# Optimization experiments

Hardware: AMD Instinct MI355X
Metric: run time of the kernel (lower is better)

## Reference

```python
import jax, jax.numpy as jnp
import numpy as np

LOG_2PI = 1.8378770664093453  # log(2*pi)


def setup_inputs() -> dict:
    key = jax.random.key(0)
    k1, k2 = jax.random.split(key)
    # Pij: posteriors [B, K, H, W]; positive like softmax outputs
    Pij = jax.random.uniform(k1, (4, 16, 512, 512), dtype=jnp.float32)
    # I: image [B, C=3, H, W]
    I = jax.random.uniform(k2, (4, 3, 512, 512), dtype=jnp.float32)
    return {"Pij": Pij, "I": I}


def reference(Pij, I):
    eps = 1e-5
    B, K, H, W = Pij.shape
    D = I.shape[1]  # = 3 (module hard-codes eye(3) jitter)
    Npix = H * W

    # M-step: mixture weights, per-class weighted means and covariances
    SP = jnp.sum(Pij, axis=(2, 3))            # [B, K]
    alpha = SP / Npix                          # [B, K]
    denom = (eps + SP)[..., None]              # [B, K, 1]
    mu = jnp.einsum('bchw,bkhw->bkc', I, Pij) / denom  # [B, K, D]

    # centered pixels per class: [B, K, D, H, W]
    diff = I[:, None, :, :, :] - mu[..., None, None]
    sig = jnp.einsum('bkhw,bkchw,bkdhw->bkcd', Pij, diff, diff) / denom[..., None]
    sig = sig + 1e-3 * jnp.eye(D, dtype=sig.dtype)  # jitter, matches eps_sigma

    # E-step: Gaussian log-density per pixel per class (tiny 3x3 algebra)
    siginv = jnp.linalg.inv(sig)               # [B, K, D, D]
    logdet = jnp.linalg.slogdet(sig)[1]        # [B, K]
    quad = jnp.einsum('bkchw,bkcd,bkdhw->bkhw', diff, siginv, diff)  # [B,K,H,W]
    logp = -0.5 * (D * LOG_2PI + logdet[..., None, None] + quad)

    Qij = alpha[..., None, None] * jnp.exp(logp)          # [B, K, H, W]
    Pij_new = Qij / (eps + jnp.sum(Qij, axis=1, keepdims=True))
    return Pij_new
```

## Files before the change

kernel.cpp:

```cpp
#include <hip/hip_runtime.h>
#include <math.h>

#define NPIX (512 * 512)
#define KCLS 16
#define NB   4
#define EPSF 1e-5f
#define D_LOG_2PI 1.8378770664093453

__global__ __launch_bounds__(256)
void k_stats(const float* __restrict__ P, const float* __restrict__ I,
             double* __restrict__ stats) {
    const int tid  = threadIdx.x;
    const int b    = blockIdx.y;
    const int base = blockIdx.x * 2048;
    const float* Ib = I + (size_t)b * 3 * NPIX;

    float xr[2][4], yr[2][4], zr[2][4];
#pragma unroll
    for (int it = 0; it < 2; ++it) {
        const int px = base + it * 1024 + tid * 4;
        *(float4*)xr[it] = *(const float4*)(Ib + px);
        *(float4*)yr[it] = *(const float4*)(Ib + NPIX + px);
        *(float4*)zr[it] = *(const float4*)(Ib + 2 * NPIX + px);
    }

    __shared__ float red[4][10];
    const int wave = tid >> 6, lane = tid & 63;

    for (int k = 0; k < KCLS; ++k) {
        const float* Pk = P + (size_t)(b * KCLS + k) * NPIX + base;
        float s[10];
#pragma unroll
        for (int j = 0; j < 10; ++j) s[j] = 0.f;

#pragma unroll
        for (int it = 0; it < 2; ++it) {
            float pv[4];
            *(float4*)pv = *(const float4*)(Pk + it * 1024 + tid * 4);
#pragma unroll
            for (int j = 0; j < 4; ++j) {
                const float p = pv[j];
                const float x = xr[it][j], y = yr[it][j], z = zr[it][j];
                const float px_ = p * x, py_ = p * y, pz_ = p * z;
                s[0] += p;
                s[1] += px_;      s[2] += py_;      s[3] += pz_;
                s[4] += px_ * x;  s[5] += px_ * y;  s[6] += px_ * z;
                s[7] += py_ * y;  s[8] += py_ * z;  s[9] += pz_ * z;
            }
        }
#pragma unroll
        for (int j = 0; j < 10; ++j) {
            float v = s[j];
#pragma unroll
            for (int off = 32; off > 0; off >>= 1)
                v += __shfl_down(v, off);
            if (lane == 0) red[wave][j] = v;
        }
        __syncthreads();
        if (tid < 10) {
            const float v = red[0][tid] + red[1][tid] + red[2][tid] + red[3][tid];
            atomicAdd(&stats[(size_t)(b * KCLS + k) * 10 + tid], (double)v);
        }
        __syncthreads();
    }
}

__global__ void k_params(const double* __restrict__ stats,
                         float* __restrict__ params) {
    const int idx = threadIdx.x;
    if (idx >= NB * KCLS) return;
    const double* s = stats + (size_t)idx * 10;
    const double SP    = s[0];
    const double denom = 1e-5 + SP;
    const double alpha = SP / (double)NPIX;
    const double m0 = s[1] / denom, m1 = s[2] / denom, m2 = s[3] / denom;
    const double c00 = (s[4] - 2.0 * m0 * s[1] + m0 * m0 * SP) / denom + 1e-3;
    const double c01 = (s[5] - m0 * s[2] - m1 * s[1] + m0 * m1 * SP) / denom;
    const double c02 = (s[6] - m0 * s[3] - m2 * s[1] + m0 * m2 * SP) / denom;
    const double c11 = (s[7] - 2.0 * m1 * s[2] + m1 * m1 * SP) / denom + 1e-3;
    const double c12 = (s[8] - m1 * s[3] - m2 * s[2] + m1 * m2 * SP) / denom;
    const double c22 = (s[9] - 2.0 * m2 * s[3] + m2 * m2 * SP) / denom + 1e-3;
    const double A00 = c11 * c22 - c12 * c12;
    const double A01 = c02 * c12 - c01 * c22;
    const double A02 = c01 * c12 - c02 * c11;
    const double A11 = c00 * c22 - c02 * c02;
    const double A12 = c01 * c02 - c00 * c12;
    const double A22 = c00 * c11 - c01 * c01;
    const double det = c00 * A00 + c01 * A01 + c02 * A02;
    const double coeff = alpha * exp(-0.5 * (3.0 * D_LOG_2PI + log(det)));
    float* o = params + (size_t)idx * 10;
    o[0] = (float)m0;          o[1] = (float)m1;          o[2] = (float)m2;
    o[3] = (float)(A00 / det); o[4] = (float)(A01 / det); o[5] = (float)(A02 / det);
    o[6] = (float)(A11 / det); o[7] = (float)(A12 / det); o[8] = (float)(A22 / det);
    o[9] = (float)coeff;
}

__global__ __launch_bounds__(256)
void k_estep(const float* __restrict__ I, const float* __restrict__ params,
             float* __restrict__ out) {
    const int b = blockIdx.y;
    __shared__ float pp[KCLS * 10];
    if (threadIdx.x < KCLS * 10)
        pp[threadIdx.x] = params[b * KCLS * 10 + threadIdx.x];
    __syncthreads();

    const int px = blockIdx.x * 1024 + threadIdx.x * 4;
    const float* Ib = I + (size_t)b * 3 * NPIX;
    float x[4], y[4], z[4];
    *(float4*)x = *(const float4*)(Ib + px);
    *(float4*)y = *(const float4*)(Ib + NPIX + px);
    *(float4*)z = *(const float4*)(Ib + 2 * NPIX + px);

    float q[KCLS][4];
    float sum[4] = {0.f, 0.f, 0.f, 0.f};
#pragma unroll
    for (int k = 0; k < KCLS; ++k) {
        const float m0  = pp[k * 10 + 0], m1  = pp[k * 10 + 1], m2  = pp[k * 10 + 2];
        const float i00 = pp[k * 10 + 3], i01 = pp[k * 10 + 4], i02 = pp[k * 10 + 5];
        const float i11 = pp[k * 10 + 6], i12 = pp[k * 10 + 7], i22 = pp[k * 10 + 8];
        const float cf  = pp[k * 10 + 9];
#pragma unroll
        for (int j = 0; j < 4; ++j) {
            const float d0 = x[j] - m0, d1 = y[j] - m1, d2 = z[j] - m2;
            const float quad = i00 * d0 * d0 + i11 * d1 * d1 + i22 * d2 * d2
                             + 2.f * (i01 * d0 * d1 + i02 * d0 * d2 + i12 * d1 * d2);
            const float qv = cf * __expf(-0.5f * quad);
            q[k][j] = qv;
            sum[j] += qv;
        }
    }
    float inv[4];
#pragma unroll
    for (int j = 0; j < 4; ++j) inv[j] = 1.f / (EPSF + sum[j]);
#pragma unroll
    for (int k = 0; k < KCLS; ++k) {
        float4 o;
        o.x = q[k][0] * inv[0];
        o.y = q[k][1] * inv[1];
        o.z = q[k][2] * inv[2];
        o.w = q[k][3] * inv[3];
        *(float4*)(out + (size_t)(b * KCLS + k) * NPIX + px) = o;
    }
}

extern "C" void kernel_launch(void* const* d_in, const int* in_sizes, int n_in,
                              void* d_out, int out_size, void* d_ws, size_t ws_size,
                              hipStream_t stream) {
    const float* Pij = (const float*)d_in[0];
    const float* I   = (const float*)d_in[1];
    float* out = (float*)d_out;

    double* stats = (double*)d_ws;
    float* params = (float*)((char*)d_ws + NB * KCLS * 10 * sizeof(double));

    hipMemsetAsync(stats, 0, NB * KCLS * 10 * sizeof(double), stream);

    k_stats <<<dim3(NPIX / 2048, NB), 256, 0, stream>>>(Pij, I, stats);
    k_params<<<1, 64, 0, stream>>>(stats, params);
    k_estep <<<dim3(NPIX / 1024, NB), 256, 0, stream>>>(I, params, out);
}
```

Baseline: 173.6 us.

## Parallelize stats kernel over (batch, class) with larger per-block pixel chunks

The stats kernel now gives each block one (batch, class) pair and an 8192-pixel chunk, where before each block looped over all 16 classes for a 2048-pixel chunk. This removes the per-class block-wide syncs and per-class reductions inside one block, and spreads the class work across more independent blocks. In exchange, the image channels are reloaded once per class, which adds image traffic that the L2 cache has to absorb.

```diff
diff --git a/kernel.cpp b/kernel.cpp
--- a/kernel.cpp
+++ b/kernel.cpp
@@ -11,57 +11,50 @@
 void k_stats(const float* __restrict__ P, const float* __restrict__ I,
              double* __restrict__ stats) {
     const int tid  = threadIdx.x;
-    const int b    = blockIdx.y;
-    const int base = blockIdx.x * 2048;
-    const float* Ib = I + (size_t)b * 3 * NPIX;
+    const int bk   = blockIdx.y;
+    const int b    = bk >> 4;
+    const int base = blockIdx.x * 8192;
+    const float* Pk = P + (size_t)bk * NPIX + base;
+    const float* Ib = I + (size_t)b * 3 * NPIX + base;
 
-    float xr[2][4], yr[2][4], zr[2][4];
+    float s[10];
 #pragma unroll
-    for (int it = 0; it < 2; ++it) {
-        const int px = base + it * 1024 + tid * 4;
-        *(float4*)xr[it] = *(const float4*)(Ib + px);
-        *(float4*)yr[it] = *(const float4*)(Ib + NPIX + px);
-        *(float4*)zr[it] = *(const float4*)(Ib + 2 * NPIX + px);
+    for (int j = 0; j < 10; ++j) s[j] = 0.f;
+
+#pragma unroll
+    for (int it = 0; it < 8; ++it) {
+        const int off = it * 1024 + tid * 4;
+        float pv[4], xv[4], yv[4], zv[4];
+        *(float4*)pv = *(const float4*)(Pk + off);
+        *(float4*)xv = *(const float4*)(Ib + off);
+        *(float4*)yv = *(const float4*)(Ib + NPIX + off);
+        *(float4*)zv = *(const float4*)(Ib + 2 * NPIX + off);
+#pragma unroll
+        for (int j = 0; j < 4; ++j) {
+            const float p = pv[j];
+            const float x = xv[j], y = yv[j], z = zv[j];
+            const float px_ = p * x, py_ = p * y, pz_ = p * z;
+            s[0] += p;
+            s[1] += px_;      s[2] += py_;      s[3] += pz_;
+            s[4] += px_ * x;  s[5] += px_ * y;  s[6] += px_ * z;
+            s[7] += py_ * y;  s[8] += py_ * z;  s[9] += pz_ * z;
+        }
     }
 
     __shared__ float red[4][10];
     const int wave = tid >> 6, lane = tid & 63;
-
-    for (int k = 0; k < KCLS; ++k) {
-        const float* Pk = P + (size_t)(b * KCLS + k) * NPIX + base;
-        float s[10];
 #pragma unroll
-        for (int j = 0; j < 10; ++j) s[j] = 0.f;
-
+    for (int j = 0; j < 10; ++j) {
+        float v = s[j];
 #pragma unroll
-        for (int it = 0; it < 2; ++it) {
-            float pv[4];
-            *(float4*)pv = *(const float4*)(Pk + it * 1024 + tid * 4);
-#pragma unroll
-            for (int j = 0; j < 4; ++j) {
-                const float p = pv[j];
-                const float x = xr[it][j], y = yr[it][j], z = zr[it][j];
-                const float px_ = p * x, py_ = p * y, pz_ = p * z;
-                s[0] += p;
-                s[1] += px_;      s[2] += py_;      s[3] += pz_;
-                s[4] += px_ * x;  s[5] += px_ * y;  s[6] += px_ * z;
-                s[7] += py_ * y;  s[8] += py_ * z;  s[9] += pz_ * z;
-            }
-        }
-#pragma unroll
-        for (int j = 0; j < 10; ++j) {
-            float v = s[j];
-#pragma unroll
-            for (int off = 32; off > 0; off >>= 1)
-                v += __shfl_down(v, off);
-            if (lane == 0) red[wave][j] = v;
-        }
-        __syncthreads();
-        if (tid < 10) {
-            const float v = red[0][tid] + red[1][tid] + red[2][tid] + red[3][tid];
-            atomicAdd(&stats[(size_t)(b * KCLS + k) * 10 + tid], (double)v);
-        }
-        __syncthreads();
+        for (int off = 32; off > 0; off >>= 1)
+            v += __shfl_down(v, off);
+        if (lane == 0) red[wave][j] = v;
+    }
+    __syncthreads();
+    if (tid < 10) {
+        const float v = red[0][tid] + red[1][tid] + red[2][tid] + red[3][tid];
+        atomicAdd(&stats[(size_t)bk * 10 + tid], (double)v);
     }
 }
 
@@ -155,7 +148,7 @@
 
     hipMemsetAsync(stats, 0, NB * KCLS * 10 * sizeof(double), stream);
 
-    k_stats <<<dim3(NPIX / 2048, NB), 256, 0, stream>>>(Pij, I, stats);
+    k_stats <<<dim3(32, NB * KCLS), 256, 0, stream>>>(Pij, I, stats);
     k_params<<<1, 64, 0, stream>>>(stats, params);
     k_estep <<<dim3(NPIX / 1024, NB), 256, 0, stream>>>(I, params, out);
 }
```

Measured after the change: 140.7 us. 19.0% less time.

## Split stats work across class groups and recompute densities in E-step

Applied to the files above, without the earlier changes.

The stats kernel now gives each block a 4096-pixel chunk and a group of 4 classes, with the grid extended over class groups. This raises memory-level parallelism and cuts the serial per-class loop with its syncs, at the cost of reloading the image once per class group. The E-step no longer keeps 64 q values in registers. It recomputes the Gaussian density in a second pass, trading twice the exp and quadratic work for lower register pressure and higher occupancy.

```diff
diff --git a/kernel.cpp b/kernel.cpp
--- a/kernel.cpp
+++ b/kernel.cpp
@@ -11,46 +11,54 @@
 void k_stats(const float* __restrict__ P, const float* __restrict__ I,
              double* __restrict__ stats) {
     const int tid  = threadIdx.x;
-    const int b    = blockIdx.y;
-    const int base = blockIdx.x * 2048;
-    const float* Ib = I + (size_t)b * 3 * NPIX;
+    const int kg   = blockIdx.y;
+    const int b    = blockIdx.z;
+    const int base = blockIdx.x * 4096;
+    const float* Ib = I + (size_t)b * 3 * NPIX + base;
 
-    float xr[2][4], yr[2][4], zr[2][4];
+    float xv[4][4], yv[4][4], zv[4][4];
 #pragma unroll
-    for (int it = 0; it < 2; ++it) {
-        const int px = base + it * 1024 + tid * 4;
-        *(float4*)xr[it] = *(const float4*)(Ib + px);
-        *(float4*)yr[it] = *(const float4*)(Ib + NPIX + px);
-        *(float4*)zr[it] = *(const float4*)(Ib + 2 * NPIX + px);
+    for (int it = 0; it < 4; ++it) {
+        const int off = it * 1024 + tid * 4;
+        *(float4*)xv[it] = *(const float4*)(Ib + off);
+        *(float4*)yv[it] = *(const float4*)(Ib + NPIX + off);
+        *(float4*)zv[it] = *(const float4*)(Ib + 2 * NPIX + off);
     }
 
-    __shared__ float red[4][10];
-    const int wave = tid >> 6, lane = tid & 63;
-
-    for (int k = 0; k < KCLS; ++k) {
-        const float* Pk = P + (size_t)(b * KCLS + k) * NPIX + base;
-        float s[10];
+    float s[4][10];
 #pragma unroll
-        for (int j = 0; j < 10; ++j) s[j] = 0.f;
+    for (int kk = 0; kk < 4; ++kk)
+#pragma unroll
+        for (int j = 0; j < 10; ++j) s[kk][j] = 0.f;
 
 #pragma unroll
-        for (int it = 0; it < 2; ++it) {
+    for (int kk = 0; kk < 4; ++kk) {
+        const int k = kg * 4 + kk;
+        const float* Pk = P + (size_t)(b * KCLS + k) * NPIX + base;
+#pragma unroll
+        for (int it = 0; it < 4; ++it) {
             float pv[4];
             *(float4*)pv = *(const float4*)(Pk + it * 1024 + tid * 4);
 #pragma unroll
             for (int j = 0; j < 4; ++j) {
                 const float p = pv[j];
-                const float x = xr[it][j], y = yr[it][j], z = zr[it][j];
+                const float x = xv[it][j], y = yv[it][j], z = zv[it][j];
                 const float px_ = p * x, py_ = p * y, pz_ = p * z;
-                s[0] += p;
-                s[1] += px_;      s[2] += py_;      s[3] += pz_;
-                s[4] += px_ * x;  s[5] += px_ * y;  s[6] += px_ * z;
-                s[7] += py_ * y;  s[8] += py_ * z;  s[9] += pz_ * z;
+                s[kk][0] += p;
+                s[kk][1] += px_;      s[kk][2] += py_;      s[kk][3] += pz_;
+                s[kk][4] += px_ * x;  s[kk][5] += px_ * y;  s[kk][6] += px_ * z;
+                s[kk][7] += py_ * y;  s[kk][8] += py_ * z;  s[kk][9] += pz_ * z;
             }
         }
+    }
+
+    __shared__ float red[4][10];
+    const int wave = tid >> 6, lane = tid & 63;
+#pragma unroll
+    for (int kk = 0; kk < 4; ++kk) {
 #pragma unroll
         for (int j = 0; j < 10; ++j) {
-            float v = s[j];
+            float v = s[kk][j];
 #pragma unroll
             for (int off = 32; off > 0; off >>= 1)
                 v += __shfl_down(v, off);
@@ -59,7 +67,7 @@
         __syncthreads();
         if (tid < 10) {
             const float v = red[0][tid] + red[1][tid] + red[2][tid] + red[3][tid];
-            atomicAdd(&stats[(size_t)(b * KCLS + k) * 10 + tid], (double)v);
+            atomicAdd(&stats[(size_t)((b * KCLS + kg * 4 + kk) * 10 + tid)], (double)v);
         }
         __syncthreads();
     }
@@ -111,7 +119,6 @@
     *(float4*)y = *(const float4*)(Ib + NPIX + px);
     *(float4*)z = *(const float4*)(Ib + 2 * NPIX + px);
 
-    float q[KCLS][4];
     float sum[4] = {0.f, 0.f, 0.f, 0.f};
 #pragma unroll
     for (int k = 0; k < KCLS; ++k) {
@@ -124,21 +131,28 @@
             const float d0 = x[j] - m0, d1 = y[j] - m1, d2 = z[j] - m2;
             const float quad = i00 * d0 * d0 + i11 * d1 * d1 + i22 * d2 * d2
                              + 2.f * (i01 * d0 * d1 + i02 * d0 * d2 + i12 * d1 * d2);
-            const float qv = cf * __expf(-0.5f * quad);
-            q[k][j] = qv;
-            sum[j] += qv;
+            sum[j] += cf * __expf(-0.5f * quad);
         }
     }
     float inv[4];
 #pragma unroll
     for (int j = 0; j < 4; ++j) inv[j] = 1.f / (EPSF + sum[j]);
+
 #pragma unroll
     for (int k = 0; k < KCLS; ++k) {
+        const float m0  = pp[k * 10 + 0], m1  = pp[k * 10 + 1], m2  = pp[k * 10 + 2];
+        const float i00 = pp[k * 10 + 3], i01 = pp[k * 10 + 4], i02 = pp[k * 10 + 5];
+        const float i11 = pp[k * 10 + 6], i12 = pp[k * 10 + 7], i22 = pp[k * 10 + 8];
+        const float cf  = pp[k * 10 + 9];
         float4 o;
-        o.x = q[k][0] * inv[0];
-        o.y = q[k][1] * inv[1];
-        o.z = q[k][2] * inv[2];
-        o.w = q[k][3] * inv[3];
+        float* ov = (float*)&o;
+#pragma unroll
+        for (int j = 0; j < 4; ++j) {
+            const float d0 = x[j] - m0, d1 = y[j] - m1, d2 = z[j] - m2;
+            const float quad = i00 * d0 * d0 + i11 * d1 * d1 + i22 * d2 * d2
+                             + 2.f * (i01 * d0 * d1 + i02 * d0 * d2 + i12 * d1 * d2);
+            ov[j] = cf * __expf(-0.5f * quad) * inv[j];
+        }
         *(float4*)(out + (size_t)(b * KCLS + k) * NPIX + px) = o;
     }
 }
@@ -155,7 +169,7 @@
 
     hipMemsetAsync(stats, 0, NB * KCLS * 10 * sizeof(double), stream);
 
-    k_stats <<<dim3(NPIX / 2048, NB), 256, 0, stream>>>(Pij, I, stats);
+    k_stats <<<dim3(64, KCLS / 4, NB), 256, 0, stream>>>(Pij, I, stats);
     k_params<<<1, 64, 0, stream>>>(stats, params);
     k_estep <<<dim3(NPIX / 1024, NB), 256, 0, stream>>>(I, params, out);
 }
```

New measurement: 147.2 us. 1.18x faster.
